# Performance work log

Measured on AMD Instinct MI355X. Metric: run time of the kernel, lower is better.

The kernel has to match this reference:

```python
import jax, jax.numpy as jnp
import numpy as np

B, S, D, H = 2, 1024, 768, 12
HD = D // H          # head_dim = 64
DFF = 4 * D          # 3072
EPS = 1e-5


def _ln(x, g, b):
    m = x.mean(-1, keepdims=True)
    v = ((x - m) ** 2).mean(-1, keepdims=True)
    return (x - m) * jax.lax.rsqrt(v + EPS) * g + b


def setup_inputs() -> dict:
    key = jax.random.key(0)
    ks = jax.random.split(key, 8)
    w = lambda k, shape: jax.random.normal(k, shape, jnp.float32) * 0.02
    return {
        "inp": jax.random.normal(ks[0], (B, S, D), jnp.float32),
        "attention_mask": jnp.zeros((B, S), bool),  # True = masked out (filled with -inf)
        "rel_matrix": jax.random.randint(ks[1], (B, S, S), -1, 2, jnp.int32),  # values in {-1,0,1}
        "qkv_w": w(ks[2], (3 * D, D)),
        "rel_A": w(ks[3], (3, HD)),        # relative_position_emb_A.weight
        "o_w": w(ks[4], (D, D)),
        "w1": w(ks[5], (DFF, D)), "b1": jnp.zeros((DFF,), jnp.float32),
        "w2": w(ks[6], (D, DFF)), "b2": jnp.zeros((D,), jnp.float32),
        "ln1_g": jnp.ones((D,), jnp.float32), "ln1_b": jnp.zeros((D,), jnp.float32),
        "ln2_g": jnp.ones((D,), jnp.float32), "ln2_b": jnp.zeros((D,), jnp.float32),
    }


def reference(inp, attention_mask, rel_matrix, qkv_w, rel_A, o_w,
              w1, b1, w2, b2, ln1_g, ln1_b, ln2_g, ln2_b):
    x = _ln(inp, ln1_g, ln1_b)
    qkv = x @ qkv_w.T                                  # (B,S,3D)
    q, k, v = jnp.split(qkv, 3, axis=-1)
    heads = lambda t: t.reshape(B, S, H, HD).transpose(0, 2, 1, 3)  # (B,H,S,HD)
    q, k, v = heads(q), heads(k), heads(v)

    # q @ (k + rel_emb)^T without materializing k_aug:
    # q.k^T term plus per-(q,key) relative term gathered from q @ A^T.
    logits = jnp.einsum("bhqd,bhkd->bhqk", q, k)       # (B,H,S,S)
    r = jnp.einsum("bhqd,cd->bhqc", q, rel_A)          # (B,H,S,3)
    idx = (rel_matrix + 1).astype(jnp.int32)           # (B,S,S) in {0,1,2}
    rel = jnp.take_along_axis(r, jnp.broadcast_to(idx[:, None], (B, H, S, S)), axis=-1)
    logits = (logits + rel) / np.sqrt(HD).astype(np.float32)
    # masked_fill: -inf where mask is True
    logits = jnp.where(attention_mask[:, None, None, :], -jnp.inf, logits)

    attn = jax.nn.softmax(logits, axis=-1)
    out = jnp.einsum("bhqk,bhkd->bhqd", attn, v)
    out = out.transpose(0, 2, 1, 3).reshape(B, S, D)
    inp = inp + out @ o_w.T                            # residual (dropout=0)

    h = _ln(inp, ln2_g, ln2_b)
    mlp = jax.nn.relu(h @ w1.T + b1) @ w2.T + b2
    return inp + mlp
```

## Files before the change

kernel.cpp:

```cpp
#include <hip/hip_runtime.h>
#include <hip/hip_bf16.h>

#define BB 2
#define SS 1024
#define DD 768
#define HH 12
#define HD 64
#define DFF 3072
#define EPS 1e-5f
#define BS2 (BB * SS)
#define BSD ((size_t)BS2 * DD)

typedef unsigned short ushort_t;
typedef unsigned char uchar_t;
using short8 = __attribute__((ext_vector_type(8))) short;
using f32x4  = __attribute__((ext_vector_type(4))) float;

#define WAITCNT_LGKM0 0xC07F

__device__ __forceinline__ ushort_t f2bf_rne(float f) {
    union { float f; unsigned u; } x; x.f = f;
    unsigned r = x.u + 0x7fff + ((x.u >> 16) & 1);
    return (ushort_t)(r >> 16);
}
__device__ __forceinline__ float bf2f(short u) {
    union { unsigned i; float f; } x;
    x.i = ((unsigned)(ushort_t)u) << 16;
    return x.f;
}
__device__ __forceinline__ short8 mergeo(short8 a, short8 b, float inv) {
    short8 o;
#pragma unroll
    for (int i = 0; i < 8; ++i)
        o[i] = (short)f2bf_rne((bf2f(a[i]) + bf2f(b[i])) * inv);
    return o;
}

#define CVT_N1 (3 * DD * DD / 4)
#define CVT_N2 (CVT_N1 + DD * DD / 4)
#define CVT_N3 (CVT_N2 + DFF * DD / 4)
#define CVT_NT (CVT_N3 + DD * DFF / 4)
#define PREP_CVT   (CVT_NT / 256)
#define PREP_CODES (BB * SS)
#define PREP_LN    BS2

__global__ __launch_bounds__(256) void prep_kernel(
    const float* __restrict__ qkv_w, const float* __restrict__ o_w,
    const float* __restrict__ w1, const float* __restrict__ w2,
    ushort_t* __restrict__ wdst,
    const int* __restrict__ rel, const uchar_t* __restrict__ mask,
    unsigned* __restrict__ codes,
    const float* __restrict__ x, const float* __restrict__ g,
    const float* __restrict__ b, ushort_t* __restrict__ y)
{
    const int bx = blockIdx.x;
    const int t  = threadIdx.x;
    if (bx < PREP_CVT) {
        int i = bx * 256 + t;
        const float* src; int off;
        if (i < CVT_N1)      { src = qkv_w; off = i; }
        else if (i < CVT_N2) { src = o_w;   off = i - CVT_N1; }
        else if (i < CVT_N3) { src = w1;    off = i - CVT_N2; }
        else                 { src = w2;    off = i - CVT_N3; }
        float4 v = ((const float4*)src)[off];
        ushort4 o;
        o.x = f2bf_rne(v.x); o.y = f2bf_rne(v.y);
        o.z = f2bf_rne(v.z); o.w = f2bf_rne(v.w);
        ((ushort4*)wdst)[i] = o;
        return;
    }
    if (bx < PREP_CVT + PREP_CODES) {
        int tid = (bx - PREP_CVT) * 256 + t;
        int l15 = tid & 15;
        int kt  = (tid >> 4) & 15;
        int q   = (tid >> 8) & (SS - 1);
        int bb  = tid >> 18;
        const int* rrow = rel + ((size_t)(bb * SS + q)) * SS + kt * 64 + l15;
        const uchar_t* mrow = mask + (size_t)bb * SS + kt * 64 + l15;
        unsigned o = 0;
#pragma unroll
        for (int nt = 0; nt < 4; ++nt) {
            unsigned c = mrow[nt * 16] ? 3u : (unsigned)(rrow[nt * 16] + 1);
            o |= c << (8 * nt);
        }
        codes[((size_t)(bb * SS + q) * 16 + kt) * 16 + l15] = o;
        return;
    }
    const int row = bx - PREP_CVT - PREP_CODES;
    const float* xr = x + (size_t)row * DD;
    float s = 0.f, ss = 0.f;
    for (int i = t; i < DD; i += 256) {
        float v = xr[i];
        s += v; ss += v * v;
    }
    for (int off = 32; off; off >>= 1) {
        s  += __shfl_down(s,  off);
        ss += __shfl_down(ss, off);
    }
    __shared__ float reds[4], redss[4], bc[2];
    if ((t & 63) == 0) { reds[t >> 6] = s; redss[t >> 6] = ss; }
    __syncthreads();
    if (t == 0) {
        float S1 = reds[0] + reds[1] + reds[2] + reds[3];
        float S2 = redss[0] + redss[1] + redss[2] + redss[3];
        float mean = S1 / DD;
        float var = S2 / DD - mean * mean;
        bc[0] = mean;
        bc[1] = rsqrtf(var + EPS);
    }
    __syncthreads();
    float mean = bc[0], inv = bc[1];
    ushort_t* yr = y + (size_t)row * DD;
    for (int i = t; i < DD; i += 256) {
        yr[i] = f2bf_rne((xr[i] - mean) * inv * g[i] + b[i]);
    }
}

__global__ __launch_bounds__(256) void merge2_ln_kernel(
    const ushort_t* __restrict__ part, const float* __restrict__ inp,
    const float* __restrict__ g, const float* __restrict__ b,
    const float* __restrict__ b2,
    float* __restrict__ outp, ushort_t* __restrict__ h_bf)
{
    const int row = blockIdx.x;
    const int t = threadIdx.x;
    float4 v = make_float4(0.f, 0.f, 0.f, 0.f);
    const size_t idx = (size_t)row * (DD / 4) + t;
    if (t < DD / 4) {
        v = ((const float4*)inp)[idx];
        ushort4 p0 = ((const ushort4*)part)[idx];
        ushort4 p1 = ((const ushort4*)(part + BSD))[idx];
        v.x += bf2f(p0.x) + bf2f(p1.x);
        v.y += bf2f(p0.y) + bf2f(p1.y);
        v.z += bf2f(p0.z) + bf2f(p1.z);
        v.w += bf2f(p0.w) + bf2f(p1.w);
        float4 b2v = ((const float4*)b2)[t];
        float4 o;
        o.x = v.x + b2v.x; o.y = v.y + b2v.y;
        o.z = v.z + b2v.z; o.w = v.w + b2v.w;
        ((float4*)outp)[idx] = o;
    }
    float s  = v.x + v.y + v.z + v.w;
    float ss = v.x * v.x + v.y * v.y + v.z * v.z + v.w * v.w;
    for (int off = 32; off; off >>= 1) {
        s  += __shfl_down(s,  off);
        ss += __shfl_down(ss, off);
    }
    __shared__ float reds[4], redss[4], bc[2];
    if ((t & 63) == 0) { reds[t >> 6] = s; redss[t >> 6] = ss; }
    __syncthreads();
    if (t == 0) {
        float S1 = reds[0] + reds[1] + reds[2] + reds[3];
        float S2 = redss[0] + redss[1] + redss[2] + redss[3];
        float mean = S1 / DD;
        float var = S2 / DD - mean * mean;
        bc[0] = mean;
        bc[1] = rsqrtf(var + EPS);
    }
    __syncthreads();
    if (t < DD / 4) {
        const float mean = bc[0], inv = bc[1];
        float4 gv = ((const float4*)g)[t];
        float4 bv = ((const float4*)b)[t];
        ushort4 o;
        o.x = f2bf_rne((v.x - mean) * inv * gv.x + bv.x);
        o.y = f2bf_rne((v.y - mean) * inv * gv.y + bv.y);
        o.z = f2bf_rne((v.z - mean) * inv * gv.z + bv.z);
        o.w = f2bf_rne((v.w - mean) * inv * gv.w + bv.w);
        ((ushort4*)h_bf)[idx] = o;
    }
}

template <bool RELU, bool OUT_BF16, bool HAS_BIAS, bool PARTIAL, bool ATOMIC, bool FUSE_ATT>
__global__ __launch_bounds__(256) void gemm_tile(
    const ushort_t* __restrict__ A, const ushort_t* __restrict__ W,
    const float* __restrict__ bias, void* __restrict__ Cout,
    const float* __restrict__ lpart,
    int M, int N, int K, int Ksplit, int nx)
{
    __shared__ __align__(16) ushort_t As[512 * 8];
    __shared__ __align__(16) ushort_t Bs[1024 * 8];

    const int nwg = gridDim.x;
    const int swz = (blockIdx.x & 7) * (nwg >> 3) + (blockIdx.x >> 3);
    const int by  = swz & 31;
    const int t2  = swz >> 5;
    const int bxx = t2 % nx;
    const int bz  = t2 / nx;

    const int t  = threadIdx.x;
    const int n0 = bxx * 128;
    const int m0 = by * 64;
    const int kb = bz * Ksplit;
    const int w  = t >> 6;
    const int l  = t & 63;
    const int wm = (w & 1) * 32;
    const int wn = (w >> 1) * 64;
    const int l15  = l & 15;
    const int quad = l >> 4;

    const ushort_t* gA = A + (size_t)(m0 + (t & 63)) * K + kb + (t >> 6) * 8;
    const ushort_t* gB = W + (size_t)(n0 + (t & 127)) * K + kb + (t >> 7) * 8;

    const float* lp0 = nullptr; const float* lp1 = nullptr;
    const int hbase = kb >> 6;
    if (FUSE_ATT) {
        lp0 = lpart + (size_t)(m0 + (t & 63)) * HH;
        lp1 = lp0 + (size_t)BS2 * HH;
    }

    short8 pa0, pa1, ra0, ra1, sa0, sa1;
    float li0 = 0.f, li1 = 0.f;
    if (FUSE_ATT) {
        ra0 = *(const short8*)(gA);
        ra1 = *(const short8*)(gA + 32);
        sa0 = *(const short8*)(gA + BSD);
        sa1 = *(const short8*)(gA + BSD + 32);
        li0 = lp0[hbase];
        li1 = lp1[hbase];
    } else {
        pa0 = *(const short8*)(gA);
        pa1 = *(const short8*)(gA + 32);
    }
    short8 pb0 = *(const short8*)(gB);
    short8 pb1 = *(const short8*)(gB + 16);
    short8 pb2 = *(const short8*)(gB + 32);
    short8 pb3 = *(const short8*)(gB + 48);

    f32x4 acc[2][4] = {};
    const int nIter = Ksplit >> 6;

    for (int it = 0; it < nIter; ++it) {
        __builtin_amdgcn_s_barrier();
        if (FUSE_ATT) {
            const float inv = 1.0f / (li0 + li1);
            pa0 = mergeo(ra0, sa0, inv);
            pa1 = mergeo(ra1, sa1, inv);
        }
        *(short8*)&As[(size_t)t * 8]           = pa0;
        *(short8*)&As[(size_t)(t + 256) * 8]   = pa1;
        *(short8*)&Bs[(size_t)t * 8]           = pb0;
        *(short8*)&Bs[(size_t)(t + 256) * 8]   = pb1;
        *(short8*)&Bs[(size_t)(t + 512) * 8]   = pb2;
        *(short8*)&Bs[(size_t)(t + 768) * 8]   = pb3;
        if (it + 1 < nIter) {
            const int k0 = (it + 1) << 6;
            if (FUSE_ATT) {
                ra0 = *(const short8*)(gA + k0);
                ra1 = *(const short8*)(gA + k0 + 32);
                sa0 = *(const short8*)(gA + k0 + BSD);
                sa1 = *(const short8*)(gA + k0 + BSD + 32);
                li0 = lp0[hbase + it + 1];
                li1 = lp1[hbase + it + 1];
            } else {
                pa0 = *(const short8*)(gA + k0);
                pa1 = *(const short8*)(gA + k0 + 32);
            }
            pb0 = *(const short8*)(gB + k0);
            pb1 = *(const short8*)(gB + k0 + 16);
            pb2 = *(const short8*)(gB + k0 + 32);
            pb3 = *(const short8*)(gB + k0 + 48);
        }
        __builtin_amdgcn_s_waitcnt(WAITCNT_LGKM0);
        __builtin_amdgcn_s_barrier();

#pragma unroll
        for (int ks = 0; ks < 2; ++ks) {
            const ushort_t* aptr = &As[(size_t)((ks * 4 + quad) * 64 + wm + l15) * 8];
            const ushort_t* bptr = &Bs[(size_t)((ks * 4 + quad) * 128 + wn + l15) * 8];
            short8 af[2], bf[4];
#pragma unroll
            for (int i = 0; i < 2; ++i)
                af[i] = *(const short8*)(aptr + (size_t)i * 16 * 8);
#pragma unroll
            for (int j = 0; j < 4; ++j)
                bf[j] = *(const short8*)(bptr + (size_t)j * 16 * 8);
#pragma unroll
            for (int i = 0; i < 2; ++i)
#pragma unroll
                for (int j = 0; j < 4; ++j)
                    acc[i][j] = __builtin_amdgcn_mfma_f32_16x16x32_bf16(
                        af[i], bf[j], acc[i][j], 0, 0, 0);
        }
    }

    if (PARTIAL) {
        ushort_t* Cp = (ushort_t*)Cout + (size_t)bz * ((size_t)M * N);
#pragma unroll
        for (int i = 0; i < 2; ++i) {
            const int row = m0 + wm + i * 16 + quad * 4;
#pragma unroll
            for (int j = 0; j < 4; ++j) {
                const int col = n0 + wn + j * 16 + l15;
#pragma unroll
                for (int r = 0; r < 4; ++r)
                    Cp[(size_t)(row + r) * N + col] = f2bf_rne(acc[i][j][r]);
            }
        }
    } else if (ATOMIC) {
        float* Cp = (float*)Cout;
#pragma unroll
        for (int i = 0; i < 2; ++i) {
            const int row = m0 + wm + i * 16 + quad * 4;
#pragma unroll
            for (int j = 0; j < 4; ++j) {
                const int col = n0 + wn + j * 16 + l15;
#pragma unroll
                for (int r = 0; r < 4; ++r)
                    atomicAdd(&Cp[(size_t)(row + r) * N + col], acc[i][j][r]);
            }
        }
    } else {
#pragma unroll
        for (int i = 0; i < 2; ++i) {
            const int row = m0 + wm + i * 16 + quad * 4;
#pragma unroll
            for (int j = 0; j < 4; ++j) {
                const int col = n0 + wn + j * 16 + l15;
                const float bv = HAS_BIAS ? bias[col] : 0.f;
#pragma unroll
                for (int r = 0; r < 4; ++r) {
                    float v = acc[i][j][r] + bv;
                    if (RELU) v = fmaxf(v, 0.f);
                    if (OUT_BF16)
                        ((ushort_t*)Cout)[(size_t)(row + r) * N + col] = f2bf_rne(v);
                    else
                        ((float*)Cout)[(size_t)(row + r) * N + col] = v;
                }
            }
        }
    }
}

__global__ __launch_bounds__(256) void attn_mfma_kernel(
    const ushort_t* __restrict__ qkv,
    const unsigned* __restrict__ codes,
    const float* __restrict__ rel_A,
    ushort_t* __restrict__ Opart,
    float* __restrict__ lpart)
{
    __shared__ __align__(16) ushort_t Ks[2][64 * 64];
    __shared__ __align__(16) unsigned Vt2[2][64 * 36];
    __shared__ __align__(16) ushort_t Ps[64 * 72];
    __shared__ __align__(16) float r3s[64][4];

    const int bx = blockIdx.x;
    const int ks = bx & 1;
    const int qt = (bx >> 1) & 15;
    const int h  = (bx >> 5) % HH;
    const int b  = bx / (32 * HH);
    const int q0 = qt * 64;
    const int t  = threadIdx.x;
    const int w  = t >> 6;
    const int l  = t & 63;
    const int l15  = l & 15;
    const int quad = l >> 4;

    const int sr  = t >> 3;
    const int scp = t & 7;
    const int vkp = t >> 3;
    const int vdg = t & 7;
    const int vkps = vkp ^ (vdg * 4);

    const size_t qrow = (size_t)(b * SS + q0 + w * 16 + l15) * (3 * DD) + h * HD;
    const short8 qf0 = *(const short8*)(qkv + qrow + quad * 8);
    const short8 qf1 = *(const short8*)(qkv + qrow + 32 + quad * 8);

    {
        float rv[3];
#pragma unroll
        for (int c = 0; c < 3; ++c) {
            const float* a = rel_A + c * HD + quad * 8;
            float acc = 0.f;
#pragma unroll
            for (int j = 0; j < 8; ++j) acc += bf2f(qf0[j]) * a[j];
#pragma unroll
            for (int j = 0; j < 8; ++j) acc += bf2f(qf1[j]) * a[32 + j];
            acc += __shfl_xor(acc, 16);
            acc += __shfl_xor(acc, 32);
            rv[c] = acc;
        }
        if (quad == 0) {
            float4 f4 = make_float4(rv[0], rv[1], rv[2], -2.4e31f);
            *(float4*)&r3s[w * 16 + l15][0] = f4;
        }
    }

    float l_run[4] = {0.f, 0.f, 0.f, 0.f};
    f32x4 oacc[4] = {};

    const int kt0 = ks * 8;
    short8 va, vb;
    {
        const int k0 = kt0 * 64;
        const int cl  = scp ^ (sr & 7);
        const ushort_t* g = qkv + (size_t)(b * SS + k0 + sr) * (3 * DD) + DD + h * HD + cl * 8;
        __builtin_amdgcn_global_load_lds(
            (const __attribute__((address_space(1))) unsigned*)g,
            (__attribute__((address_space(3))) unsigned*)(&Ks[0][0] + (size_t)t * 8), 16, 0, 0);
        const int r2  = sr + 32;
        const int cl2 = scp ^ (r2 & 7);
        const ushort_t* g2 = qkv + (size_t)(b * SS + k0 + r2) * (3 * DD) + DD + h * HD + cl2 * 8;
        __builtin_amdgcn_global_load_lds(
            (const __attribute__((address_space(1))) unsigned*)g2,
            (__attribute__((address_space(3))) unsigned*)(&Ks[0][0] + (size_t)(t + 256) * 8), 16, 0, 0);
        const ushort_t* gv = qkv + (size_t)(b * SS + k0 + 2 * vkp) * (3 * DD) + 2 * DD + h * HD + vdg * 8;
        va = *(const short8*)gv;
        vb = *(const short8*)(gv + 3 * DD);
#pragma unroll
        for (int i = 0; i < 8; ++i)
            Vt2[0][(size_t)(vdg * 8 + i) * 36 + vkps] =
                (unsigned)(ushort_t)va[i] | ((unsigned)(ushort_t)vb[i] << 16);
    }
    __syncthreads();
    float4 r3v[4];
#pragma unroll
    for (int reg = 0; reg < 4; ++reg)
        r3v[reg] = *(const float4*)&r3s[w * 16 + quad * 4 + reg][0];

    for (int i8 = 0; i8 < 8; ++i8) {
        const int kt  = kt0 + i8;
        const int cur = i8 & 1;
        const bool more = (i8 + 1 < 8);
        if (more) {
            const int k0 = (kt + 1) * 64;
            const int nb = cur ^ 1;
            const int cl  = scp ^ (sr & 7);
            const ushort_t* g = qkv + (size_t)(b * SS + k0 + sr) * (3 * DD) + DD + h * HD + cl * 8;
            __builtin_amdgcn_global_load_lds(
                (const __attribute__((address_space(1))) unsigned*)g,
                (__attribute__((address_space(3))) unsigned*)(&Ks[nb][0] + (size_t)t * 8), 16, 0, 0);
            const int r2  = sr + 32;
            const int cl2 = scp ^ (r2 & 7);
            const ushort_t* g2 = qkv + (size_t)(b * SS + k0 + r2) * (3 * DD) + DD + h * HD + cl2 * 8;
            __builtin_amdgcn_global_load_lds(
                (const __attribute__((address_space(1))) unsigned*)g2,
                (__attribute__((address_space(3))) unsigned*)(&Ks[nb][0] + (size_t)(t + 256) * 8), 16, 0, 0);
            const ushort_t* gv = qkv + (size_t)(b * SS + k0 + 2 * vkp) * (3 * DD) + 2 * DD + h * HD + vdg * 8;
            va = *(const short8*)gv;
            vb = *(const short8*)(gv + 3 * DD);
        }

        f32x4 sacc[4] = {};
#pragma unroll
        for (int kc = 0; kc < 2; ++kc) {
            const short8 qv = kc ? qf1 : qf0;
#pragma unroll
            for (int nt = 0; nt < 4; ++nt) {
                const int row = nt * 16 + l15;
                const int cp  = (kc * 4 + quad) ^ (row & 7);
                const short8 kf = *(const short8*)(&Ks[cur][0] + (size_t)row * 64 + cp * 8);
                sacc[nt] = __builtin_amdgcn_mfma_f32_16x16x32_bf16(qv, kf, sacc[nt], 0, 0, 0);
            }
        }

#pragma unroll
        for (int reg = 0; reg < 4; ++reg) {
            const int qloc = w * 16 + quad * 4 + reg;
            const unsigned cds = codes[((size_t)(b * SS + q0 + qloc) * 16 + kt) * 16 + l15];
            const float4 r4 = r3v[reg];
#pragma unroll
            for (int nt = 0; nt < 4; ++nt) {
                const unsigned c = (cds >> (8 * nt)) & 0xff;
                float rvv = (c == 0) ? r4.x : (c == 1) ? r4.y : (c == 2) ? r4.z : r4.w;
                const float p = __expf((sacc[nt][reg] + rvv) * 0.125f);
                l_run[reg] += p;
                Ps[(size_t)qloc * 72 + nt * 16 + l15] = f2bf_rne(p);
            }
        }

#pragma unroll
        for (int kc = 0; kc < 2; ++kc) {
            const short8 pf = *(const short8*)(Ps + (size_t)(w * 16 + l15) * 72 + kc * 32 + quad * 8);
#pragma unroll
            for (int dt = 0; dt < 4; ++dt) {
                const int d  = dt * 16 + l15;
                const int dg = d >> 3;
                const int kps0 = (kc * 16 + quad * 4) ^ ((dg & 7) * 4);
                const short8 vf = *(const short8*)((const ushort_t*)&Vt2[cur][(size_t)d * 36 + kps0]);
                oacc[dt] = __builtin_amdgcn_mfma_f32_16x16x32_bf16(pf, vf, oacc[dt], 0, 0, 0);
            }
        }

        if (more) {
            const int nb = cur ^ 1;
#pragma unroll
            for (int i = 0; i < 8; ++i)
                Vt2[nb][(size_t)(vdg * 8 + i) * 36 + vkps] =
                    (unsigned)(ushort_t)va[i] | ((unsigned)(ushort_t)vb[i] << 16);
            __syncthreads();
        }
    }

    ushort_t* Op = Opart + (size_t)ks * BSD;
    float* lp = lpart + (size_t)ks * BS2 * HH;
#pragma unroll
    for (int reg = 0; reg < 4; ++reg) {
        float ls = l_run[reg];
        ls += __shfl_xor(ls, 1);
        ls += __shfl_xor(ls, 2);
        ls += __shfl_xor(ls, 4);
        ls += __shfl_xor(ls, 8);
        const int orow = b * SS + q0 + w * 16 + quad * 4 + reg;
#pragma unroll
        for (int dt = 0; dt < 4; ++dt)
            Op[(size_t)orow * DD + h * HD + dt * 16 + l15] = f2bf_rne(oacc[dt][reg]);
        if (l15 == 0) lp[(size_t)orow * HH + h] = ls;
    }
}

extern "C" void kernel_launch(void* const* d_in, const int* in_sizes, int n_in,
                              void* d_out, int out_size, void* d_ws, size_t ws_size,
                              hipStream_t stream) {
    const float* inp   = (const float*)d_in[0];
    const uchar_t* amask = (const uchar_t*)d_in[1];
    const int*   relm  = (const int*)d_in[2];
    const float* qkv_w = (const float*)d_in[3];
    const float* rel_A = (const float*)d_in[4];
    const float* o_w   = (const float*)d_in[5];
    const float* w1    = (const float*)d_in[6];
    const float* b1    = (const float*)d_in[7];
    const float* w2    = (const float*)d_in[8];
    const float* b2    = (const float*)d_in[9];
    const float* ln1_g = (const float*)d_in[10];
    const float* ln1_b = (const float*)d_in[11];
    const float* ln2_g = (const float*)d_in[12];
    const float* ln2_b = (const float*)d_in[13];
    float* out = (float*)d_out;

    char* p = (char*)d_ws;
    ushort_t* x_bf   = (ushort_t*)p; p += BSD * 2;
    ushort_t* h_bf   = (ushort_t*)p; p += BSD * 2;
    ushort_t* ff_bf  = (ushort_t*)p; p += (size_t)BS2 * DFF * 2;
    ushort_t* qkvw_bf= (ushort_t*)p; p += (size_t)3 * DD * DD * 2;
    ushort_t* ow_bf  = (ushort_t*)p; p += (size_t)DD * DD * 2;
    ushort_t* w1_bf  = (ushort_t*)p; p += (size_t)DFF * DD * 2;
    ushort_t* w2_bf  = (ushort_t*)p; p += (size_t)DD * DFF * 2;
    ushort_t* qkv_bf = (ushort_t*)p; p += (size_t)BS2 * 3 * DD * 2;
    ushort_t* pool   = (ushort_t*)p; p += 4 * BSD * 2;
    ushort_t* Opart  = (ushort_t*)p; p += 2 * BSD * 2;
    float*    lpart  = (float*)p;    p += (size_t)2 * BS2 * HH * 4;
    unsigned* codes  = (unsigned*)p; p += (size_t)BB * SS * SS;

    prep_kernel<<<PREP_CVT + PREP_CODES + PREP_LN, 256, 0, stream>>>(
        qkv_w, o_w, w1, w2, qkvw_bf, relm, amask, codes,
        inp, ln1_g, ln1_b, x_bf);

    gemm_tile<false, true, false, false, false, false>
        <<<3 * DD / 128 * 32, 256, 0, stream>>>(
        x_bf, qkvw_bf, nullptr, qkv_bf, nullptr, BS2, 3 * DD, DD, DD, 3 * DD / 128);

    attn_mfma_kernel<<<BB * HH * 16 * 2, 256, 0, stream>>>(
        qkv_bf, codes, rel_A, Opart, lpart);

    gemm_tile<false, false, false, true, false, true>
        <<<DD / 128 * 32 * 2, 256, 0, stream>>>(
        Opart, ow_bf, nullptr, pool, lpart, BS2, DD, DD, DD / 2, DD / 128);

    merge2_ln_kernel<<<BS2, 256, 0, stream>>>(
        pool, inp, ln2_g, ln2_b, b2, out, h_bf);

    gemm_tile<true, true, true, false, false, false>
        <<<DFF / 128 * 32, 256, 0, stream>>>(
        h_bf, w1_bf, b1, ff_bf, nullptr, BS2, DFF, DD, DD, DFF / 128);

    gemm_tile<false, false, false, false, true, false>
        <<<DD / 128 * 32 * 4, 256, 0, stream>>>(
        ff_bf, w2_bf, nullptr, out, nullptr, BS2, DD, DFF, DFF / 4, DD / 128);
}
```

Before: 263.5 us.

## Co-schedule prep work with QKV GEMM and attention; replace atomic split-K with bf16 partial merge

The monolithic prep kernel is split up. Only the QKV weight conversion and LN1 run first. The rel/mask code packing now runs as extra blocks in the QKV GEMM launch, and the remaining weight conversions (o_w, w1, w2) run as extra blocks in the attention launch, so this memory-bound work can fill idle CUs alongside compute kernels. The FFN2 split-K no longer uses fp32 atomicAdd into the output. It writes four bf16 partials to a pool, and a new merge kernel adds them with the residual and b2. This trades atomic traffic for an extra launch and extra partial reads/writes, and adds bf16 rounding of the partials.

```diff
diff --git a/kernel.cpp b/kernel.cpp
--- a/kernel.cpp
+++ b/kernel.cpp
@@ -36,57 +36,31 @@
     return o;
 }
 
-#define CVT_N1 (3 * DD * DD / 4)
-#define CVT_N2 (CVT_N1 + DD * DD / 4)
-#define CVT_N3 (CVT_N2 + DFF * DD / 4)
-#define CVT_NT (CVT_N3 + DD * DFF / 4)
-#define PREP_CVT   (CVT_NT / 256)
-#define PREP_CODES (BB * SS)
-#define PREP_LN    BS2
-
-__global__ __launch_bounds__(256) void prep_kernel(
-    const float* __restrict__ qkv_w, const float* __restrict__ o_w,
-    const float* __restrict__ w1, const float* __restrict__ w2,
-    ushort_t* __restrict__ wdst,
-    const int* __restrict__ rel, const uchar_t* __restrict__ mask,
-    unsigned* __restrict__ codes,
+__device__ __forceinline__ void cvt_quad(const float* __restrict__ src, int off,
+                                         ushort_t* __restrict__ dst, int i) {
+    float4 v = ((const float4*)src)[off];
+    ushort4 o;
+    o.x = f2bf_rne(v.x); o.y = f2bf_rne(v.y);
+    o.z = f2bf_rne(v.z); o.w = f2bf_rne(v.w);
+    ((ushort4*)dst)[i] = o;
+}
+
+#define P1_CVT (3 * DD * DD / 4 / 256)
+#define P1_LN  BS2
+
+__global__ __launch_bounds__(256) void prep1_kernel(
+    const float* __restrict__ qkv_w, ushort_t* __restrict__ qkvw_bf,
     const float* __restrict__ x, const float* __restrict__ g,
     const float* __restrict__ b, ushort_t* __restrict__ y)
 {
     const int bx = blockIdx.x;
     const int t  = threadIdx.x;
-    if (bx < PREP_CVT) {
+    if (bx < P1_CVT) {
         int i = bx * 256 + t;
-        const float* src; int off;
-        if (i < CVT_N1)      { src = qkv_w; off = i; }
-        else if (i < CVT_N2) { src = o_w;   off = i - CVT_N1; }
-        else if (i < CVT_N3) { src = w1;    off = i - CVT_N2; }
-        else                 { src = w2;    off = i - CVT_N3; }
-        float4 v = ((const float4*)src)[off];
-        ushort4 o;
-        o.x = f2bf_rne(v.x); o.y = f2bf_rne(v.y);
-        o.z = f2bf_rne(v.z); o.w = f2bf_rne(v.w);
-        ((ushort4*)wdst)[i] = o;
+        cvt_quad(qkv_w, i, qkvw_bf, i);
         return;
     }
-    if (bx < PREP_CVT + PREP_CODES) {
-        int tid = (bx - PREP_CVT) * 256 + t;
-        int l15 = tid & 15;
-        int kt  = (tid >> 4) & 15;
-        int q   = (tid >> 8) & (SS - 1);
-        int bb  = tid >> 18;
-        const int* rrow = rel + ((size_t)(bb * SS + q)) * SS + kt * 64 + l15;
-        const uchar_t* mrow = mask + (size_t)bb * SS + kt * 64 + l15;
-        unsigned o = 0;
-#pragma unroll
-        for (int nt = 0; nt < 4; ++nt) {
-            unsigned c = mrow[nt * 16] ? 3u : (unsigned)(rrow[nt * 16] + 1);
-            o |= c << (8 * nt);
-        }
-        codes[((size_t)(bb * SS + q) * 16 + kt) * 16 + l15] = o;
-        return;
-    }
-    const int row = bx - PREP_CVT - PREP_CODES;
+    const int row = bx - P1_CVT;
     const float* xr = x + (size_t)row * DD;
     float s = 0.f, ss = 0.f;
     for (int i = t; i < DD; i += 256) {
@@ -119,8 +93,7 @@
 __global__ __launch_bounds__(256) void merge2_ln_kernel(
     const ushort_t* __restrict__ part, const float* __restrict__ inp,
     const float* __restrict__ g, const float* __restrict__ b,
-    const float* __restrict__ b2,
-    float* __restrict__ outp, ushort_t* __restrict__ h_bf)
+    float* __restrict__ resid, ushort_t* __restrict__ h_bf)
 {
     const int row = blockIdx.x;
     const int t = threadIdx.x;
@@ -134,11 +107,7 @@
         v.y += bf2f(p0.y) + bf2f(p1.y);
         v.z += bf2f(p0.z) + bf2f(p1.z);
         v.w += bf2f(p0.w) + bf2f(p1.w);
-        float4 b2v = ((const float4*)b2)[t];
-        float4 o;
-        o.x = v.x + b2v.x; o.y = v.y + b2v.y;
-        o.z = v.z + b2v.z; o.w = v.w + b2v.w;
-        ((float4*)outp)[idx] = o;
+        ((float4*)resid)[idx] = v;
     }
     float s  = v.x + v.y + v.z + v.w;
     float ss = v.x * v.x + v.y * v.y + v.z * v.z + v.w * v.w;
@@ -171,8 +140,28 @@
     }
 }
 
-template <bool RELU, bool OUT_BF16, bool HAS_BIAS, bool PARTIAL, bool ATOMIC, bool FUSE_ATT>
-__global__ __launch_bounds__(256) void gemm_tile(
+__global__ __launch_bounds__(256) void merge4_kernel(
+    const ushort_t* __restrict__ part, const float* __restrict__ resid,
+    const float* __restrict__ b2, float* __restrict__ outp, int n4)
+{
+    int i = blockIdx.x * 256 + threadIdx.x;
+    if (i >= n4) return;
+    float4 v = ((const float4*)resid)[i];
+    int col4 = (i * 4) % DD;
+    float4 bv = *(const float4*)(b2 + col4);
+    v.x += bv.x; v.y += bv.y; v.z += bv.z; v.w += bv.w;
+#pragma unroll
+    for (int z = 0; z < 4; ++z) {
+        ushort4 pz = ((const ushort4*)(part + (size_t)z * BSD))[i];
+        v.x += bf2f(pz.x); v.y += bf2f(pz.y);
+        v.z += bf2f(pz.z); v.w += bf2f(pz.w);
+    }
+    ((float4*)outp)[i] = v;
+}
+
+template <bool RELU, bool OUT_BF16, bool HAS_BIAS, bool PARTIAL, bool FUSE_ATT>
+__device__ __forceinline__ void gemm_body(
+    int bid, int nwg,
     const ushort_t* __restrict__ A, const ushort_t* __restrict__ W,
     const float* __restrict__ bias, void* __restrict__ Cout,
     const float* __restrict__ lpart,
@@ -181,8 +170,7 @@
     __shared__ __align__(16) ushort_t As[512 * 8];
     __shared__ __align__(16) ushort_t Bs[1024 * 8];
 
-    const int nwg = gridDim.x;
-    const int swz = (blockIdx.x & 7) * (nwg >> 3) + (blockIdx.x >> 3);
+    const int swz = (bid & 7) * (nwg >> 3) + (bid >> 3);
     const int by  = swz & 31;
     const int t2  = swz >> 5;
     const int bxx = t2 % nx;
@@ -297,19 +285,6 @@
                     Cp[(size_t)(row + r) * N + col] = f2bf_rne(acc[i][j][r]);
             }
         }
-    } else if (ATOMIC) {
-        float* Cp = (float*)Cout;
-#pragma unroll
-        for (int i = 0; i < 2; ++i) {
-            const int row = m0 + wm + i * 16 + quad * 4;
-#pragma unroll
-            for (int j = 0; j < 4; ++j) {
-                const int col = n0 + wn + j * 16 + l15;
-#pragma unroll
-                for (int r = 0; r < 4; ++r)
-                    atomicAdd(&Cp[(size_t)(row + r) * N + col], acc[i][j][r]);
-            }
-        }
     } else {
 #pragma unroll
         for (int i = 0; i < 2; ++i) {
@@ -332,25 +307,86 @@
     }
 }
 
-__global__ __launch_bounds__(256) void attn_mfma_kernel(
+template <bool RELU, bool OUT_BF16, bool HAS_BIAS, bool PARTIAL, bool FUSE_ATT>
+__global__ __launch_bounds__(256) void gemm_tile(
+    const ushort_t* __restrict__ A, const ushort_t* __restrict__ W,
+    const float* __restrict__ bias, void* __restrict__ Cout,
+    const float* __restrict__ lpart,
+    int M, int N, int K, int Ksplit, int nx)
+{
+    gemm_body<RELU, OUT_BF16, HAS_BIAS, PARTIAL, FUSE_ATT>(
+        blockIdx.x, gridDim.x, A, W, bias, Cout, lpart, M, N, K, Ksplit, nx);
+}
+
+#define QKV_G (3 * DD / 128 * 32)
+
+__global__ __launch_bounds__(256) void qkv_codes_kernel(
+    const ushort_t* __restrict__ A, const ushort_t* __restrict__ W,
+    ushort_t* __restrict__ Cout,
+    const int* __restrict__ rel, const uchar_t* __restrict__ mask,
+    unsigned* __restrict__ codes)
+{
+    const int bx = blockIdx.x;
+    if (bx < QKV_G) {
+        gemm_body<false, true, false, false, false>(
+            bx, QKV_G, A, W, nullptr, Cout, nullptr,
+            BS2, 3 * DD, DD, DD, 3 * DD / 128);
+        return;
+    }
+    const int t = threadIdx.x;
+    int tid = (bx - QKV_G) * 256 + t;
+    int l15 = tid & 15;
+    int kt  = (tid >> 4) & 15;
+    int q   = (tid >> 8) & (SS - 1);
+    int bb  = tid >> 18;
+    const int* rrow = rel + ((size_t)(bb * SS + q)) * SS + kt * 64 + l15;
+    const uchar_t* mrow = mask + (size_t)bb * SS + kt * 64 + l15;
+    unsigned o = 0;
+#pragma unroll
+    for (int nt = 0; nt < 4; ++nt) {
+        unsigned c = mrow[nt * 16] ? 3u : (unsigned)(rrow[nt * 16] + 1);
+        o |= c << (8 * nt);
+    }
+    codes[((size_t)(bb * SS + q) * 16 + kt) * 16 + l15] = o;
+}
+
+#define ATT_G (BB * HH * 16 * 2)
+#define RC1 (DD * DD / 4)
+#define RC2 (RC1 + DFF * DD / 4)
+#define RCT (RC2 + DD * DFF / 4)
+#define RCVT_BLK (RCT / 256)
+
+__global__ __launch_bounds__(256) void attn_cvt_kernel(
     const ushort_t* __restrict__ qkv,
     const unsigned* __restrict__ codes,
     const float* __restrict__ rel_A,
     ushort_t* __restrict__ Opart,
-    float* __restrict__ lpart)
+    float* __restrict__ lpart,
+    const float* __restrict__ o_w, const float* __restrict__ w1,
+    const float* __restrict__ w2, ushort_t* __restrict__ wrest)
 {
+    const int bx = blockIdx.x;
+    const int t  = threadIdx.x;
+    if (bx >= ATT_G) {
+        int i = (bx - ATT_G) * 256 + t;
+        const float* src; int off;
+        if (i < RC1)      { src = o_w; off = i; }
+        else if (i < RC2) { src = w1;  off = i - RC1; }
+        else              { src = w2;  off = i - RC2; }
+        cvt_quad(src, off, wrest, i);
+        return;
+    }
+
     __shared__ __align__(16) ushort_t Ks[2][64 * 64];
     __shared__ __align__(16) unsigned Vt2[2][64 * 36];
     __shared__ __align__(16) ushort_t Ps[64 * 72];
     __shared__ __align__(16) float r3s[64][4];
 
-    const int bx = blockIdx.x;
     const int ks = bx & 1;
     const int qt = (bx >> 1) & 15;
     const int h  = (bx >> 5) % HH;
     const int b  = bx / (32 * HH);
     const int q0 = qt * 64;
-    const int t  = threadIdx.x;
     const int w  = t >> 6;
     const int l  = t & 63;
     const int l15  = l & 15;
@@ -537,34 +573,36 @@
     ushort_t* w1_bf  = (ushort_t*)p; p += (size_t)DFF * DD * 2;
     ushort_t* w2_bf  = (ushort_t*)p; p += (size_t)DD * DFF * 2;
     ushort_t* qkv_bf = (ushort_t*)p; p += (size_t)BS2 * 3 * DD * 2;
+    float*    resid  = (float*)p;    p += BSD * 4;
     ushort_t* pool   = (ushort_t*)p; p += 4 * BSD * 2;
     ushort_t* Opart  = (ushort_t*)p; p += 2 * BSD * 2;
     float*    lpart  = (float*)p;    p += (size_t)2 * BS2 * HH * 4;
     unsigned* codes  = (unsigned*)p; p += (size_t)BB * SS * SS;
 
-    prep_kernel<<<PREP_CVT + PREP_CODES + PREP_LN, 256, 0, stream>>>(
-        qkv_w, o_w, w1, w2, qkvw_bf, relm, amask, codes,
-        inp, ln1_g, ln1_b, x_bf);
-
-    gemm_tile<false, true, false, false, false, false>
-        <<<3 * DD / 128 * 32, 256, 0, stream>>>(
-        x_bf, qkvw_bf, nullptr, qkv_bf, nullptr, BS2, 3 * DD, DD, DD, 3 * DD / 128);
-
-    attn_mfma_kernel<<<BB * HH * 16 * 2, 256, 0, stream>>>(
-        qkv_bf, codes, rel_A, Opart, lpart);
-
-    gemm_tile<false, false, false, true, false, true>
+    prep1_kernel<<<P1_CVT + P1_LN, 256, 0, stream>>>(
+        qkv_w, qkvw_bf, inp, ln1_g, ln1_b, x_bf);
+
+    qkv_codes_kernel<<<QKV_G + BB * SS, 256, 0, stream>>>(
+        x_bf, qkvw_bf, qkv_bf, relm, amask, codes);
+
+    attn_cvt_kernel<<<ATT_G + RCVT_BLK, 256, 0, stream>>>(
+        qkv_bf, codes, rel_A, Opart, lpart, o_w, w1, w2, ow_bf);
+
+    gemm_tile<false, false, false, true, true>
         <<<DD / 128 * 32 * 2, 256, 0, stream>>>(
         Opart, ow_bf, nullptr, pool, lpart, BS2, DD, DD, DD / 2, DD / 128);
 
     merge2_ln_kernel<<<BS2, 256, 0, stream>>>(
-        pool, inp, ln2_g, ln2_b, b2, out, h_bf);
-
-    gemm_tile<true, true, true, false, false, false>
+        pool, inp, ln2_g, ln2_b, resid, h_bf);
+
+    gemm_tile<true, true, true, false, false>
         <<<DFF / 128 * 32, 256, 0, stream>>>(
         h_bf, w1_bf, b1, ff_bf, nullptr, BS2, DFF, DD, DD, DFF / 128);
 
-    gemm_tile<false, false, false, false, true, false>
+    gemm_tile<false, false, false, true, false>
         <<<DD / 128 * 32 * 4, 256, 0, stream>>>(
-        ff_bf, w2_bf, nullptr, out, nullptr, BS2, DD, DFF, DFF / 4, DD / 128);
-}
+        ff_bf, w2_bf, nullptr, pool, nullptr, BS2, DD, DFF, DFF / 4, DD / 128);
+
+    merge4_kernel<<<(int)(BSD / 4 / 256), 256, 0, stream>>>(
+        pool, resid, b2, out, (int)(BSD / 4));
+}
```

New measurement: 253.8 us. 3.7% less time.
